# Optimization experiments

Hardware: AMD Instinct MI355X
Metric: run time of the kernel (lower is better)

Reference implementation:

```python
import jax, jax.numpy as jnp
import numpy as np

TEMPERATURE = 0.5
EPS = 1e-8  # matches F.cosine_similarity eps clamp


def setup_inputs() -> dict:
    key = jax.random.key(0)
    k1, k2 = jax.random.split(key)
    logits = jax.random.normal(k1, (8192, 256), dtype=jnp.float32)
    label = jax.random.randint(k2, (8192,), 0, 10, dtype=jnp.int64)
    return {"logits": logits, "label": label}


def reference(logits, label):
    n = label.shape[0]
    # pairwise cosine similarity via normalize + GEMM (same math as the
    # broadcasted F.cosine_similarity, without the O(n^2 d) intermediate)
    norms = jnp.maximum(jnp.linalg.norm(logits, axis=1, keepdims=True), EPS)
    xn = logits / norms                       # [n, d]
    sim_matrix = xn @ xn.T                    # [n, n]

    eye = jnp.eye(n, dtype=sim_matrix.dtype)
    mask = (label[:, None] == label[None, :]).astype(sim_matrix.dtype)  # same-label (incl. diag)

    e = jnp.exp(sim_matrix / TEMPERATURE) * (1.0 - eye)  # zero diagonal
    sim = mask * e                            # same-label positives
    no_sim_sum = jnp.sum(e - sim, axis=1)     # [n] row sums of different-label terms
    sim_sum = sim + no_sim_sum[:, None]       # denominator per entry
    ratio = sim / sim_sum

    # zeros (different-label entries) get +1 via (1 - mask), diagonal gets +1 via eye -> -log(1) = 0
    loss_mat = -jnp.log((1.0 - mask) + ratio + eye)
    return jnp.sum(loss_mat) / (2 * n)
```

## Files before the change

kernel.cpp:

```cpp
#include <hip/hip_runtime.h>
#include <cstdint>
#include <cstddef>

typedef float  f32x4  __attribute__((ext_vector_type(4)));
typedef long long i64;
typedef unsigned char uchar;

#define N_ROWS 8192
#define KDIM   256
#define TEMP_INV 2.0f
#define LOG2E  1.4426950408889634f
#define EXPC   (TEMP_INV * LOG2E)

#define AS1 __attribute__((address_space(1)))
#define AS3 __attribute__((address_space(3)))

__global__ __launch_bounds__(256) void prep(const float* __restrict__ logits,
        const int* __restrict__ label, uchar* __restrict__ xn8,
        int* __restrict__ perm, int* __restrict__ labelPerm,
        int* __restrict__ classStart, int* __restrict__ cumTiles)
{
    __shared__ int lcnt[256][10];
    __shared__ int cstart[11];
    __shared__ int ccount[10];
    const int tid = threadIdx.x;
    const int bid = blockIdx.x;

    if (bid < 2048) {
        const int p = bid * 4 + (tid >> 6);
        const int lane = tid & 63;
        float4 v = reinterpret_cast<const float4*>(logits + (size_t)p * KDIM)[lane];
        float ss = v.x*v.x + v.y*v.y + v.z*v.z + v.w*v.w;
        #pragma unroll
        for (int off = 32; off >= 1; off >>= 1) ss += __shfl_xor(ss, off, 64);
        float inv = 1.0f / fmaxf(sqrtf(ss), 1e-8f);
        int pk = __builtin_amdgcn_cvt_pk_fp8_f32(v.x * inv, v.y * inv, 0, false);
        pk     = __builtin_amdgcn_cvt_pk_fp8_f32(v.z * inv, v.w * inv, pk, true);
        reinterpret_cast<unsigned int*>(xn8 + (size_t)p * KDIM)[lane] = (unsigned int)pk;
        return;
    }

    const int wave = tid >> 6, lane = tid & 63;
    const int beg = tid * 32, end = beg + 32;
    int loc[10] = {0,0,0,0,0,0,0,0,0,0};
    for (int i = beg; i < end; ++i) {
        int c = label[i]; c = (c < 0) ? 0 : (c > 9 ? 9 : c);
        loc[c]++;
    }
    #pragma unroll
    for (int c = 0; c < 10; ++c) lcnt[tid][c] = loc[c];
    __syncthreads();

    for (int c = wave; c < 10; c += 4) {
        int s0 = lcnt[lane*4+0][c], s1 = lcnt[lane*4+1][c];
        int s2 = lcnt[lane*4+2][c], s3 = lcnt[lane*4+3][c];
        int tot = s0 + s1 + s2 + s3;
        int incl = tot;
        #pragma unroll
        for (int d = 1; d < 64; d <<= 1) {
            int up = __shfl_up(incl, d, 64);
            if (lane >= d) incl += up;
        }
        int excl = incl - tot;
        lcnt[lane*4+0][c] = excl;
        lcnt[lane*4+1][c] = excl + s0;
        lcnt[lane*4+2][c] = excl + s0 + s1;
        lcnt[lane*4+3][c] = excl + s0 + s1 + s2;
        if (lane == 63) ccount[c] = incl;
    }
    __syncthreads();

    if (tid == 0) {
        int run = 0, runT = 0;
        for (int c = 0; c < 10; ++c) {
            cstart[c] = run; classStart[c] = run;
            int tpc = (ccount[c] + 127) >> 7;
            cumTiles[c] = runT;
            run  += ccount[c];
            runT += tpc * (tpc + 1) / 2;
        }
        cstart[10] = run; classStart[10] = run; cumTiles[10] = runT;
    }
    __syncthreads();

    int ofs[10];
    #pragma unroll
    for (int c = 0; c < 10; ++c) ofs[c] = lcnt[tid][c];
    for (int i = beg; i < end; ++i) {
        int c = label[i]; c = (c < 0) ? 0 : (c > 9 ? 9 : c);
        int pos = cstart[c] + ofs[c]++;
        perm[pos] = i;
        labelPerm[pos] = c;
    }
}

__device__ __forceinline__ void stage_oneshot(const uchar* __restrict__ xn8,
        const int* __restrict__ perm, int rowBase, int colBase,
        uchar* As, uchar* Bs, int tid)
{
    const int t4 = tid >> 4;
    const int ch = (tid & 15) ^ t4;
    #pragma unroll
    for (int i = 0; i < 8; ++i) {
        const int row = i * 16 + t4;
        int rA = rowBase + row; if (rA > N_ROWS - 1) rA = N_ROWS - 1;
        int rB = colBase + row; if (rB > N_ROWS - 1) rB = N_ROWS - 1;
        const int lds_off = (i * 256 + tid) * 16;
        const uchar* gA = xn8 + (size_t)perm[rA] * KDIM + ch * 16;
        const uchar* gB = xn8 + (size_t)perm[rB] * KDIM + ch * 16;
        __builtin_amdgcn_global_load_lds((const AS1 void*)gA, (AS3 void*)(As + lds_off), 16, 0, 0);
        __builtin_amdgcn_global_load_lds((const AS1 void*)gB, (AS3 void*)(Bs + lds_off), 16, 0, 0);
    }
}

__device__ __forceinline__ void mfma_oneshot(const uchar* As, const uchar* Bs,
        f32x4 (&acc)[4][4], int wave, int lane)
{
    const int wr = wave >> 1, wc = wave & 1;
    const int lrow = lane & 15, kgrp = lane >> 4;
    const int ch2 = kgrp >> 1, half8 = (kgrp & 1) * 8;
    #pragma unroll
    for (int s = 0; s < 8; ++s) {
        const int c16 = s * 2 + ch2;
        i64 a[4], b[4];
        #pragma unroll
        for (int mi = 0; mi < 4; ++mi) {
            const int row = wr*64 + mi*16 + lrow;
            a[mi] = *reinterpret_cast<const i64*>(As + (size_t)row * 256 + ((c16 ^ lrow) * 16) + half8);
        }
        #pragma unroll
        for (int ni = 0; ni < 4; ++ni) {
            const int row = wc*64 + ni*16 + lrow;
            b[ni] = *reinterpret_cast<const i64*>(Bs + (size_t)row * 256 + ((c16 ^ lrow) * 16) + half8);
        }
        #pragma unroll
        for (int mi = 0; mi < 4; ++mi)
            #pragma unroll
            for (int ni = 0; ni < 4; ++ni)
                acc[mi][ni] = __builtin_amdgcn_mfma_f32_16x16x32_fp8_fp8(a[mi], b[ni], acc[mi][ni], 0, 0, 0);
    }
}

__global__ __launch_bounds__(256, 2) void phase1_gemm(const uchar* __restrict__ xn8,
        const int* __restrict__ perm, const int* __restrict__ labelPerm,
        float* __restrict__ pD)
{
    __shared__ __align__(16) char pool[65536];
    uchar* As = (uchar*)(pool);
    uchar* Bs = (uchar*)(pool + 32768);
    float* rowD = (float*)pool;
    float* colD = (float*)(pool + 16384);
    __shared__ int labLDS[256];

    const int tid = threadIdx.x;
    const int wave = tid >> 6, lane = tid & 63;

    int t = blockIdx.x, bi = 0;
    while (t >= 64 - bi) { t -= 64 - bi; ++bi; }
    const int bj = bi + t;
    const bool isDiag = (bi == bj);
    const int rowBase = bi * 128, colBase = bj * 128;

    if (labelPerm[rowBase] == labelPerm[colBase + 127]) {
        if (tid < 128)       pD[(size_t)bj * N_ROWS + rowBase + tid] = 0.f;
        else if (!isDiag)    pD[(size_t)bi * N_ROWS + colBase + tid - 128] = 0.f;
        return;
    }

    stage_oneshot(xn8, perm, rowBase, colBase, As, Bs, tid);
    labLDS[tid] = labelPerm[(tid < 128) ? (rowBase + tid) : (colBase + tid - 128)];
    __syncthreads();

    f32x4 acc[4][4] = {};
    mfma_oneshot(As, Bs, acc, wave, lane);
    __syncthreads();

    const int wr = wave >> 1, wc = wave & 1;
    const int lrow = lane & 15, lgrp = lane >> 4;
    float colAcc[4] = {0.f, 0.f, 0.f, 0.f};
    #pragma unroll
    for (int mi = 0; mi < 4; ++mi) {
        #pragma unroll
        for (int reg = 0; reg < 4; ++reg) {
            const int tr = wr * 64 + mi * 16 + lgrp * 4 + reg;
            const int rl = labLDS[tr];
            float rowAcc = 0.f;
            #pragma unroll
            for (int ni = 0; ni < 4; ++ni) {
                const int tc = wc * 64 + ni * 16 + lrow;
                float e = __builtin_amdgcn_exp2f(acc[mi][ni][reg] * EXPC);
                float ed = (rl != labLDS[128 + tc]) ? e : 0.f;
                rowAcc += ed;
                colAcc[ni] += ed;
            }
            rowD[tr * 32 + wc * 16 + lrow] = rowAcc;
        }
    }
    if (!isDiag) {
        #pragma unroll
        for (int ni = 0; ni < 4; ++ni) {
            const int tc = wc * 64 + ni * 16 + lrow;
            colD[tc * 8 + wr * 4 + lgrp] = colAcc[ni];
        }
    }
    __syncthreads();

    if (tid < 128) {
        const float* p = rowD + tid * 32;
        float s = 0.f;
        #pragma unroll
        for (int k = 0; k < 8; ++k) {
            f32x4 v = *reinterpret_cast<const f32x4*>(p + k * 4);
            s += v[0] + v[1] + v[2] + v[3];
        }
        pD[(size_t)bj * N_ROWS + rowBase + tid] = s;
    } else if (!isDiag) {
        const int c2 = tid - 128;
        const float* p = colD + c2 * 8;
        f32x4 v0 = *reinterpret_cast<const f32x4*>(p);
        f32x4 v1 = *reinterpret_cast<const f32x4*>(p + 4);
        pD[(size_t)bi * N_ROWS + colBase + c2] =
            v0[0] + v0[1] + v0[2] + v0[3] + v1[0] + v1[1] + v1[2] + v1[3];
    }
}

__global__ __launch_bounds__(256, 2) void phase3_loss(const uchar* __restrict__ xn8,
        const int* __restrict__ perm, const float* __restrict__ pD,
        const int* __restrict__ classStart, const int* __restrict__ cumTiles,
        float* __restrict__ partial)
{
    __shared__ __align__(16) char pool[65536];
    uchar* As = (uchar*)(pool);
    uchar* Bs = (uchar*)(pool + 32768);
    __shared__ float redF[256];
    __shared__ float DarrH[256];
    __shared__ float DarrR[128];
    __shared__ float DarrC[128];
    __shared__ int   meta[22];

    const int tid = threadIdx.x;
    const int wave = tid >> 6, lane = tid & 63;

    if (tid < 11) { meta[tid] = classStart[tid]; meta[11 + tid] = cumTiles[tid]; }
    __syncthreads();
    const int nTiles = meta[11 + 10];

    float tileSum = 0.f;
    for (int b = blockIdx.x; b < nTiles; b += 512) {
        __syncthreads();

        int c = 0;
        while (c < 9 && b >= meta[11 + c + 1]) ++c;
        const int s = meta[c], e = meta[c + 1];
        const int nc = e - s;
        const int tps = (nc + 127) >> 7;
        int lt = b - meta[11 + c];
        int ti = 0;
        while (lt >= tps - ti) { lt -= tps - ti; ++ti; }
        const int tj = ti + lt;
        const bool isDiagT = (ti == tj);
        const int rowBase = s + ti * 128, colBase = s + tj * 128;

        stage_oneshot(xn8, perm, rowBase, colBase, As, Bs, tid);

        {
            int r = rowBase + (tid & 127); if (r > N_ROWS - 1) r = N_ROWS - 1;
            const int half = tid >> 7;
            float d = 0.f;
            #pragma unroll 4
            for (int sl = half * 32; sl < half * 32 + 32; ++sl)
                d += pD[(size_t)sl * N_ROWS + r];
            DarrH[(tid & 127) * 2 + half] = d;
        }
        __syncthreads();
        if (tid < 128) DarrR[tid] = DarrH[tid * 2] + DarrH[tid * 2 + 1];
        __syncthreads();
        if (!isDiagT) {
            int r = colBase + (tid & 127); if (r > N_ROWS - 1) r = N_ROWS - 1;
            const int half = tid >> 7;
            float d = 0.f;
            #pragma unroll 4
            for (int sl = half * 32; sl < half * 32 + 32; ++sl)
                d += pD[(size_t)sl * N_ROWS + r];
            DarrH[(tid & 127) * 2 + half] = d;
            __syncthreads();
            if (tid < 128) DarrC[tid] = DarrH[tid * 2] + DarrH[tid * 2 + 1];
        }
        __syncthreads();

        f32x4 acc[4][4] = {};
        mfma_oneshot(As, Bs, acc, wave, lane);

        const int wr = wave >> 1, wc = wave & 1;
        const int lrow = lane & 15, lgrp = lane >> 4;
        #pragma unroll
        for (int mi = 0; mi < 4; ++mi) {
            #pragma unroll
            for (int reg = 0; reg < 4; ++reg) {
                const int tr = wr * 64 + mi * 16 + lgrp * 4 + reg;
                const int r = rowBase + tr;
                if (r < e) {
                    const float Dr = DarrR[tr];
                    #pragma unroll
                    for (int ni = 0; ni < 4; ++ni) {
                        const int tc = wc * 64 + ni * 16 + lrow;
                        const int cg = colBase + tc;
                        if (cg < e) {
                            float sim = acc[mi][ni][reg];
                            float ev = __builtin_amdgcn_exp2f(sim * EXPC);
                            if (isDiagT) {
                                if (cg != r)
                                    tileSum += __logf(ev + Dr) - TEMP_INV * sim;
                            } else {
                                tileSum += __logf(ev + Dr) + __logf(ev + DarrC[tc])
                                         - 2.0f * TEMP_INV * sim;
                            }
                        }
                    }
                }
            }
        }
    }

    __syncthreads();
    redF[tid] = tileSum;
    __syncthreads();
    for (int st = 128; st > 0; st >>= 1) {
        if (tid < st) redF[tid] += redF[tid + st];
        __syncthreads();
    }
    if (tid == 0) partial[blockIdx.x] = redF[0];
}

__global__ void phase4_final(const float* __restrict__ partial, float* __restrict__ out)
{
    __shared__ float red[256];
    const int tid = threadIdx.x;
    float s = partial[tid] + partial[tid + 256];
    red[tid] = s;
    __syncthreads();
    for (int st = 128; st > 0; st >>= 1) {
        if (tid < st) red[tid] += red[tid + st];
        __syncthreads();
    }
    if (tid == 0) out[0] = red[0] * (1.0f / 16384.0f);
}

extern "C" void kernel_launch(void* const* d_in, const int* in_sizes, int n_in,
                              void* d_out, int out_size, void* d_ws, size_t ws_size,
                              hipStream_t stream)
{
    const float* logits = (const float*)d_in[0];
    const int*   label  = (const int*)d_in[1];
    float* out = (float*)d_out;

    char* ws = (char*)d_ws;
    uchar*  xn8       = (uchar*)(ws);
    float*  pD        = (float*)(ws + (2u << 20));
    int*    perm      = (int*)(ws + (4u << 20));
    int*    labelPerm = (int*)(ws + (4u << 20) + (32u << 10));
    int*    classStart= (int*)(ws + (4u << 20) + (64u << 10));
    int*    cumTiles  = (int*)(ws + (4u << 20) + (64u << 10) + 256);
    float*  partial   = (float*)(ws + (4u << 20) + (128u << 10));

    hipLaunchKernelGGL(prep, dim3(2049), dim3(256), 0, stream,
                       logits, label, xn8, perm, labelPerm, classStart, cumTiles);
    hipLaunchKernelGGL(phase1_gemm, dim3(2080), dim3(256), 0, stream,
                       xn8, perm, labelPerm, pD);
    hipLaunchKernelGGL(phase3_loss, dim3(512), dim3(256), 0, stream,
                       xn8, perm, pD, classStart, cumTiles, partial);
    hipLaunchKernelGGL(phase4_final, dim3(1), dim3(256), 0, stream,
                       partial, out);
}
```

Measured before the change: 67.97 us.

## Enlarge phase1 GEMM tiles to 256x256 with 512-thread blocks

The phase1 symmetric GEMM moves from 128x128 tiles with 256 threads to 256x256 tiles with 512 threads (8 waves, each computing a 128x64 block), using 128KB of LDS per block. The grid drops from 2080 to 528 upper-triangle tiles, so pD holds 32 column slices instead of 64, and phase3 now sums 32 slices. The aim is to halve the global loads per FLOP and cut per-block overhead. In exchange, occupancy falls to one block per CU, there are fewer blocks to spread across the CUs, and the same-label skip check is coarser, so fewer tiles can be skipped.

```diff
diff --git a/kernel.cpp b/kernel.cpp
--- a/kernel.cpp
+++ b/kernel.cpp
@@ -91,6 +91,127 @@
         int pos = cstart[c] + ofs[c]++;
         perm[pos] = i;
         labelPerm[pos] = c;
+    }
+}
+
+__device__ __forceinline__ void stage_quad(const uchar* __restrict__ xn8,
+        const int* __restrict__ perm, int rowBase, int colBase,
+        uchar* As, uchar* Bs, int tid)
+{
+    const int t5 = tid >> 4;
+    const int ch = (tid & 15) ^ (t5 & 15);
+    #pragma unroll
+    for (int i = 0; i < 8; ++i) {
+        const int row = i * 32 + t5;
+        const int lds_off = (i * 512 + tid) * 16;
+        const uchar* gA = xn8 + (size_t)perm[rowBase + row] * KDIM + ch * 16;
+        const uchar* gB = xn8 + (size_t)perm[colBase + row] * KDIM + ch * 16;
+        __builtin_amdgcn_global_load_lds((const AS1 void*)gA, (AS3 void*)(As + lds_off), 16, 0, 0);
+        __builtin_amdgcn_global_load_lds((const AS1 void*)gB, (AS3 void*)(Bs + lds_off), 16, 0, 0);
+    }
+}
+
+__global__ __launch_bounds__(512, 1) void phase1_gemm(const uchar* __restrict__ xn8,
+        const int* __restrict__ perm, const int* __restrict__ labelPerm,
+        float* __restrict__ pD)
+{
+    __shared__ __align__(16) char pool[131072];
+    uchar* As = (uchar*)(pool);
+    uchar* Bs = (uchar*)(pool + 65536);
+    float* rowD = (float*)pool;
+    float* colD = (float*)(pool + 65536);
+    __shared__ int labq[512];
+
+    const int tid = threadIdx.x;
+    const int wave = tid >> 6, lane = tid & 63;
+
+    int t = blockIdx.x, Bi = 0;
+    while (t >= 32 - Bi) { t -= 32 - Bi; ++Bi; }
+    const int Bj = Bi + t;
+    const bool isDiag = (Bi == Bj);
+    const int rowBase = Bi * 256, colBase = Bj * 256;
+
+    if (labelPerm[rowBase] == labelPerm[colBase + 255]) {
+        if (tid < 256)       pD[(size_t)Bj * N_ROWS + rowBase + tid] = 0.f;
+        else if (!isDiag)    pD[(size_t)Bi * N_ROWS + colBase + tid - 256] = 0.f;
+        return;
+    }
+
+    stage_quad(xn8, perm, rowBase, colBase, As, Bs, tid);
+    labq[tid] = labelPerm[(tid < 256) ? (rowBase + tid) : (colBase + tid - 256)];
+    __syncthreads();
+
+    const int wr = wave >> 2, wc = wave & 3;
+    const int lrow = lane & 15, kgrp = lane >> 4;
+    const int ch2 = kgrp >> 1, half8 = (kgrp & 1) * 8;
+    f32x4 acc[8][4] = {};
+    #pragma unroll
+    for (int s = 0; s < 8; ++s) {
+        const int c16 = s * 2 + ch2;
+        i64 a[8], b[4];
+        #pragma unroll
+        for (int mi = 0; mi < 8; ++mi) {
+            const int row = wr*128 + mi*16 + lrow;
+            a[mi] = *reinterpret_cast<const i64*>(As + (size_t)row * 256 + ((c16 ^ lrow) * 16) + half8);
+        }
+        #pragma unroll
+        for (int ni = 0; ni < 4; ++ni) {
+            const int row = wc*64 + ni*16 + lrow;
+            b[ni] = *reinterpret_cast<const i64*>(Bs + (size_t)row * 256 + ((c16 ^ lrow) * 16) + half8);
+        }
+        #pragma unroll
+        for (int mi = 0; mi < 8; ++mi)
+            #pragma unroll
+            for (int ni = 0; ni < 4; ++ni)
+                acc[mi][ni] = __builtin_amdgcn_mfma_f32_16x16x32_fp8_fp8(a[mi], b[ni], acc[mi][ni], 0, 0, 0);
+    }
+    __syncthreads();
+
+    const int lgrp = lane >> 4;
+    float colAcc[4] = {0.f, 0.f, 0.f, 0.f};
+    #pragma unroll
+    for (int mi = 0; mi < 8; ++mi) {
+        #pragma unroll
+        for (int reg = 0; reg < 4; ++reg) {
+            const int tr = wr * 128 + mi * 16 + lgrp * 4 + reg;
+            const int rl = labq[tr];
+            float rowAcc = 0.f;
+            #pragma unroll
+            for (int ni = 0; ni < 4; ++ni) {
+                const int tc = wc * 64 + ni * 16 + lrow;
+                float e = __builtin_amdgcn_exp2f(acc[mi][ni][reg] * EXPC);
+                float ed = (rl != labq[256 + tc]) ? e : 0.f;
+                rowAcc += ed;
+                colAcc[ni] += ed;
+            }
+            rowD[tr * 64 + wc * 16 + lrow] = rowAcc;
+        }
+    }
+    if (!isDiag) {
+        #pragma unroll
+        for (int ni = 0; ni < 4; ++ni) {
+            const int tc = wc * 64 + ni * 16 + lrow;
+            colD[tc * 8 + wr * 4 + lgrp] = colAcc[ni];
+        }
+    }
+    __syncthreads();
+
+    if (tid < 256) {
+        const float* p = rowD + tid * 64;
+        float s = 0.f;
+        #pragma unroll
+        for (int k = 0; k < 16; ++k) {
+            f32x4 v = *reinterpret_cast<const f32x4*>(p + k * 4);
+            s += v[0] + v[1] + v[2] + v[3];
+        }
+        pD[(size_t)Bj * N_ROWS + rowBase + tid] = s;
+    } else if (!isDiag) {
+        const int c2 = tid - 256;
+        const float* p = colD + c2 * 8;
+        f32x4 v0 = *reinterpret_cast<const f32x4*>(p);
+        f32x4 v1 = *reinterpret_cast<const f32x4*>(p + 4);
+        pD[(size_t)Bi * N_ROWS + colBase + c2] =
+            v0[0] + v0[1] + v0[2] + v0[3] + v1[0] + v1[1] + v1[2] + v1[3];
     }
 }
 
@@ -138,89 +259,6 @@
             #pragma unroll
             for (int ni = 0; ni < 4; ++ni)
                 acc[mi][ni] = __builtin_amdgcn_mfma_f32_16x16x32_fp8_fp8(a[mi], b[ni], acc[mi][ni], 0, 0, 0);
-    }
-}
-
-__global__ __launch_bounds__(256, 2) void phase1_gemm(const uchar* __restrict__ xn8,
-        const int* __restrict__ perm, const int* __restrict__ labelPerm,
-        float* __restrict__ pD)
-{
-    __shared__ __align__(16) char pool[65536];
-    uchar* As = (uchar*)(pool);
-    uchar* Bs = (uchar*)(pool + 32768);
-    float* rowD = (float*)pool;
-    float* colD = (float*)(pool + 16384);
-    __shared__ int labLDS[256];
-
-    const int tid = threadIdx.x;
-    const int wave = tid >> 6, lane = tid & 63;
-
-    int t = blockIdx.x, bi = 0;
-    while (t >= 64 - bi) { t -= 64 - bi; ++bi; }
-    const int bj = bi + t;
-    const bool isDiag = (bi == bj);
-    const int rowBase = bi * 128, colBase = bj * 128;
-
-    if (labelPerm[rowBase] == labelPerm[colBase + 127]) {
-        if (tid < 128)       pD[(size_t)bj * N_ROWS + rowBase + tid] = 0.f;
-        else if (!isDiag)    pD[(size_t)bi * N_ROWS + colBase + tid - 128] = 0.f;
-        return;
-    }
-
-    stage_oneshot(xn8, perm, rowBase, colBase, As, Bs, tid);
-    labLDS[tid] = labelPerm[(tid < 128) ? (rowBase + tid) : (colBase + tid - 128)];
-    __syncthreads();
-
-    f32x4 acc[4][4] = {};
-    mfma_oneshot(As, Bs, acc, wave, lane);
-    __syncthreads();
-
-    const int wr = wave >> 1, wc = wave & 1;
-    const int lrow = lane & 15, lgrp = lane >> 4;
-    float colAcc[4] = {0.f, 0.f, 0.f, 0.f};
-    #pragma unroll
-    for (int mi = 0; mi < 4; ++mi) {
-        #pragma unroll
-        for (int reg = 0; reg < 4; ++reg) {
-            const int tr = wr * 64 + mi * 16 + lgrp * 4 + reg;
-            const int rl = labLDS[tr];
-            float rowAcc = 0.f;
-            #pragma unroll
-            for (int ni = 0; ni < 4; ++ni) {
-                const int tc = wc * 64 + ni * 16 + lrow;
-                float e = __builtin_amdgcn_exp2f(acc[mi][ni][reg] * EXPC);
-                float ed = (rl != labLDS[128 + tc]) ? e : 0.f;
-                rowAcc += ed;
-                colAcc[ni] += ed;
-            }
-            rowD[tr * 32 + wc * 16 + lrow] = rowAcc;
-        }
-    }
-    if (!isDiag) {
-        #pragma unroll
-        for (int ni = 0; ni < 4; ++ni) {
-            const int tc = wc * 64 + ni * 16 + lrow;
-            colD[tc * 8 + wr * 4 + lgrp] = colAcc[ni];
-        }
-    }
-    __syncthreads();
-
-    if (tid < 128) {
-        const float* p = rowD + tid * 32;
-        float s = 0.f;
-        #pragma unroll
-        for (int k = 0; k < 8; ++k) {
-            f32x4 v = *reinterpret_cast<const f32x4*>(p + k * 4);
-            s += v[0] + v[1] + v[2] + v[3];
-        }
-        pD[(size_t)bj * N_ROWS + rowBase + tid] = s;
-    } else if (!isDiag) {
-        const int c2 = tid - 128;
-        const float* p = colD + c2 * 8;
-        f32x4 v0 = *reinterpret_cast<const f32x4*>(p);
-        f32x4 v1 = *reinterpret_cast<const f32x4*>(p + 4);
-        pD[(size_t)bi * N_ROWS + colBase + c2] =
-            v0[0] + v0[1] + v0[2] + v0[3] + v1[0] + v1[1] + v1[2] + v1[3];
     }
 }
 
@@ -268,7 +306,7 @@
             const int half = tid >> 7;
             float d = 0.f;
             #pragma unroll 4
-            for (int sl = half * 32; sl < half * 32 + 32; ++sl)
+            for (int sl = half * 16; sl < half * 16 + 16; ++sl)
                 d += pD[(size_t)sl * N_ROWS + r];
             DarrH[(tid & 127) * 2 + half] = d;
         }
@@ -280,7 +318,7 @@
             const int half = tid >> 7;
             float d = 0.f;
             #pragma unroll 4
-            for (int sl = half * 32; sl < half * 32 + 32; ++sl)
+            for (int sl = half * 16; sl < half * 16 + 16; ++sl)
                 d += pD[(size_t)sl * N_ROWS + r];
             DarrH[(tid & 127) * 2 + half] = d;
             __syncthreads();
@@ -365,7 +403,7 @@
 
     hipLaunchKernelGGL(prep, dim3(2049), dim3(256), 0, stream,
                        logits, label, xn8, perm, labelPerm, classStart, cumTiles);
-    hipLaunchKernelGGL(phase1_gemm, dim3(2080), dim3(256), 0, stream,
+    hipLaunchKernelGGL(phase1_gemm, dim3(528), dim3(512), 0, stream,
                        xn8, perm, labelPerm, pD);
     hipLaunchKernelGGL(phase3_loss, dim3(512), dim3(256), 0, stream,
                        xn8, perm, pD, classStart, cumTiles, partial);
```

Result: slower. 74.07 us (+9.0%).

## Split K staging into two halves to halve LDS and raise occupancy

Applied to the files above, without the earlier changes.

The GEMM tiles in both the phase1 and phase3 kernels now stage A and B in two K-halves of 128 bytes instead of one 256-byte shot. This halves the LDS pool to 32KB and raises launch bounds from 2 to 4 blocks per CU. The swizzle changes to an 8-chunk XOR pattern to match the new row pitch. In exchange, each tile adds two extra barriers and a load phase with no overlap between them, and any latency hiding must now come from the extra resident blocks.

```diff
diff --git a/kernel.cpp b/kernel.cpp
--- a/kernel.cpp
+++ b/kernel.cpp
@@ -94,44 +94,44 @@
     }
 }
 
-__device__ __forceinline__ void stage_oneshot(const uchar* __restrict__ xn8,
-        const int* __restrict__ perm, int rowBase, int colBase,
+__device__ __forceinline__ void stage_half(const uchar* __restrict__ xn8,
+        const int* __restrict__ perm, int rowBase, int colBase, int kb,
         uchar* As, uchar* Bs, int tid)
 {
-    const int t4 = tid >> 4;
-    const int ch = (tid & 15) ^ t4;
-    #pragma unroll
-    for (int i = 0; i < 8; ++i) {
-        const int row = i * 16 + t4;
+    #pragma unroll
+    for (int i = 0; i < 4; ++i) {
+        const int ci = i * 256 + tid;
+        const int row = ci >> 3;
+        const int c = (ci & 7) ^ (row & 7);
         int rA = rowBase + row; if (rA > N_ROWS - 1) rA = N_ROWS - 1;
         int rB = colBase + row; if (rB > N_ROWS - 1) rB = N_ROWS - 1;
-        const int lds_off = (i * 256 + tid) * 16;
-        const uchar* gA = xn8 + (size_t)perm[rA] * KDIM + ch * 16;
-        const uchar* gB = xn8 + (size_t)perm[rB] * KDIM + ch * 16;
+        const int lds_off = ci * 16;
+        const uchar* gA = xn8 + (size_t)perm[rA] * KDIM + kb + c * 16;
+        const uchar* gB = xn8 + (size_t)perm[rB] * KDIM + kb + c * 16;
         __builtin_amdgcn_global_load_lds((const AS1 void*)gA, (AS3 void*)(As + lds_off), 16, 0, 0);
         __builtin_amdgcn_global_load_lds((const AS1 void*)gB, (AS3 void*)(Bs + lds_off), 16, 0, 0);
     }
 }
 
-__device__ __forceinline__ void mfma_oneshot(const uchar* As, const uchar* Bs,
+__device__ __forceinline__ void mfma_half(const uchar* As, const uchar* Bs,
         f32x4 (&acc)[4][4], int wave, int lane)
 {
     const int wr = wave >> 1, wc = wave & 1;
     const int lrow = lane & 15, kgrp = lane >> 4;
     const int ch2 = kgrp >> 1, half8 = (kgrp & 1) * 8;
     #pragma unroll
-    for (int s = 0; s < 8; ++s) {
+    for (int s = 0; s < 4; ++s) {
         const int c16 = s * 2 + ch2;
         i64 a[4], b[4];
         #pragma unroll
         for (int mi = 0; mi < 4; ++mi) {
             const int row = wr*64 + mi*16 + lrow;
-            a[mi] = *reinterpret_cast<const i64*>(As + (size_t)row * 256 + ((c16 ^ lrow) * 16) + half8);
+            a[mi] = *reinterpret_cast<const i64*>(As + (size_t)row * 128 + ((c16 ^ (row & 7)) * 16) + half8);
         }
         #pragma unroll
         for (int ni = 0; ni < 4; ++ni) {
             const int row = wc*64 + ni*16 + lrow;
-            b[ni] = *reinterpret_cast<const i64*>(Bs + (size_t)row * 256 + ((c16 ^ lrow) * 16) + half8);
+            b[ni] = *reinterpret_cast<const i64*>(Bs + (size_t)row * 128 + ((c16 ^ (row & 7)) * 16) + half8);
         }
         #pragma unroll
         for (int mi = 0; mi < 4; ++mi)
@@ -141,13 +141,13 @@
     }
 }
 
-__global__ __launch_bounds__(256, 2) void phase1_gemm(const uchar* __restrict__ xn8,
+__global__ __launch_bounds__(256, 4) void phase1_gemm(const uchar* __restrict__ xn8,
         const int* __restrict__ perm, const int* __restrict__ labelPerm,
         float* __restrict__ pD)
 {
-    __shared__ __align__(16) char pool[65536];
+    __shared__ __align__(16) char pool[32768];
     uchar* As = (uchar*)(pool);
-    uchar* Bs = (uchar*)(pool + 32768);
+    uchar* Bs = (uchar*)(pool + 16384);
     float* rowD = (float*)pool;
     float* colD = (float*)(pool + 16384);
     __shared__ int labLDS[256];
@@ -167,12 +167,16 @@
         return;
     }
 
-    stage_oneshot(xn8, perm, rowBase, colBase, As, Bs, tid);
+    stage_half(xn8, perm, rowBase, colBase, 0, As, Bs, tid);
     labLDS[tid] = labelPerm[(tid < 128) ? (rowBase + tid) : (colBase + tid - 128)];
     __syncthreads();
 
     f32x4 acc[4][4] = {};
-    mfma_oneshot(As, Bs, acc, wave, lane);
+    mfma_half(As, Bs, acc, wave, lane);
+    __syncthreads();
+    stage_half(xn8, perm, rowBase, colBase, 128, As, Bs, tid);
+    __syncthreads();
+    mfma_half(As, Bs, acc, wave, lane);
     __syncthreads();
 
     const int wr = wave >> 1, wc = wave & 1;
@@ -224,14 +228,14 @@
     }
 }
 
-__global__ __launch_bounds__(256, 2) void phase3_loss(const uchar* __restrict__ xn8,
+__global__ __launch_bounds__(256, 4) void phase3_loss(const uchar* __restrict__ xn8,
         const int* __restrict__ perm, const float* __restrict__ pD,
         const int* __restrict__ classStart, const int* __restrict__ cumTiles,
         float* __restrict__ partial)
 {
-    __shared__ __align__(16) char pool[65536];
+    __shared__ __align__(16) char pool[32768];
     uchar* As = (uchar*)(pool);
-    uchar* Bs = (uchar*)(pool + 32768);
+    uchar* Bs = (uchar*)(pool + 16384);
     __shared__ float redF[256];
     __shared__ float DarrH[256];
     __shared__ float DarrR[128];
@@ -261,7 +265,7 @@
         const bool isDiagT = (ti == tj);
         const int rowBase = s + ti * 128, colBase = s + tj * 128;
 
-        stage_oneshot(xn8, perm, rowBase, colBase, As, Bs, tid);
+        stage_half(xn8, perm, rowBase, colBase, 0, As, Bs, tid);
 
         {
             int r = rowBase + (tid & 127); if (r > N_ROWS - 1) r = N_ROWS - 1;
@@ -289,7 +293,11 @@
         __syncthreads();
 
         f32x4 acc[4][4] = {};
-        mfma_oneshot(As, Bs, acc, wave, lane);
+        mfma_half(As, Bs, acc, wave, lane);
+        __syncthreads();
+        stage_half(xn8, perm, rowBase, colBase, 128, As, Bs, tid);
+        __syncthreads();
+        mfma_half(As, Bs, acc, wave, lane);
 
         const int wr = wave >> 1, wc = wave & 1;
         const int lrow = lane & 15, lgrp = lane >> 4;
```

Result: slower. 71.56 us (+5.3%).

## Pair column tiles per block to reuse row tile and overlap staging

Applied to the files above, without the earlier changes.

Each phase1 block now handles two adjacent column tiles that share one staged row tile, halving the grid. The second B tile is loaded while the first tile's epilogue runs, and row and column partial sums are reduced with wave shuffles instead of large LDS scratch arrays. The prep label pass now uses a strided, register-cached layout, which changes the stable order within each class. The risk is fewer blocks to fill the GPU and longer serial work per block.

```diff
diff --git a/kernel.cpp b/kernel.cpp
--- a/kernel.cpp
+++ b/kernel.cpp
@@ -41,12 +41,15 @@
     }
 
     const int wave = tid >> 6, lane = tid & 63;
-    const int beg = tid * 32, end = beg + 32;
+    int lab[32];
+    #pragma unroll
+    for (int j = 0; j < 32; ++j) {
+        int c = label[tid + j * 256];
+        lab[j] = (c < 0) ? 0 : (c > 9 ? 9 : c);
+    }
     int loc[10] = {0,0,0,0,0,0,0,0,0,0};
-    for (int i = beg; i < end; ++i) {
-        int c = label[i]; c = (c < 0) ? 0 : (c > 9 ? 9 : c);
-        loc[c]++;
-    }
+    #pragma unroll
+    for (int j = 0; j < 32; ++j) loc[lab[j]]++;
     #pragma unroll
     for (int c = 0; c < 10; ++c) lcnt[tid][c] = loc[c];
     __syncthreads();
@@ -86,12 +89,166 @@
     int ofs[10];
     #pragma unroll
     for (int c = 0; c < 10; ++c) ofs[c] = lcnt[tid][c];
-    for (int i = beg; i < end; ++i) {
-        int c = label[i]; c = (c < 0) ? 0 : (c > 9 ? 9 : c);
+    #pragma unroll
+    for (int j = 0; j < 32; ++j) {
+        int c = lab[j];
         int pos = cstart[c] + ofs[c]++;
-        perm[pos] = i;
+        perm[pos] = tid + j * 256;
         labelPerm[pos] = c;
     }
+}
+
+__device__ __forceinline__ void stage_mat(const uchar* __restrict__ xn8,
+        const int* __restrict__ perm, int base, uchar* dst, int tid)
+{
+    const int t4 = tid >> 4;
+    const int ch = (tid & 15) ^ t4;
+    #pragma unroll
+    for (int i = 0; i < 8; ++i) {
+        const int row = i * 16 + t4;
+        const int lds_off = (i * 256 + tid) * 16;
+        const uchar* g = xn8 + (size_t)perm[base + row] * KDIM + ch * 16;
+        __builtin_amdgcn_global_load_lds((const AS1 void*)g, (AS3 void*)(dst + lds_off), 16, 0, 0);
+    }
+}
+
+__device__ __forceinline__ void mfma_oneshot(const uchar* As, const uchar* Bs,
+        f32x4 (&acc)[4][4], int wave, int lane)
+{
+    const int wr = wave >> 1, wc = wave & 1;
+    const int lrow = lane & 15, kgrp = lane >> 4;
+    const int ch2 = kgrp >> 1, half8 = (kgrp & 1) * 8;
+    #pragma unroll
+    for (int s = 0; s < 8; ++s) {
+        const int c16 = s * 2 + ch2;
+        i64 a[4], b[4];
+        #pragma unroll
+        for (int mi = 0; mi < 4; ++mi) {
+            const int row = wr*64 + mi*16 + lrow;
+            a[mi] = *reinterpret_cast<const i64*>(As + (size_t)row * 256 + ((c16 ^ lrow) * 16) + half8);
+        }
+        #pragma unroll
+        for (int ni = 0; ni < 4; ++ni) {
+            const int row = wc*64 + ni*16 + lrow;
+            b[ni] = *reinterpret_cast<const i64*>(Bs + (size_t)row * 256 + ((c16 ^ lrow) * 16) + half8);
+        }
+        #pragma unroll
+        for (int mi = 0; mi < 4; ++mi)
+            #pragma unroll
+            for (int ni = 0; ni < 4; ++ni)
+                acc[mi][ni] = __builtin_amdgcn_mfma_f32_16x16x32_fp8_fp8(a[mi], b[ni], acc[mi][ni], 0, 0, 0);
+    }
+}
+
+__device__ __forceinline__ void epilogue_reg(f32x4 (&acc)[4][4],
+        const int* labR, const int* labC, float (*rowHalf)[2], float (*colHalf)[2],
+        int wave, int lane)
+{
+    const int wr = wave >> 1, wc = wave & 1;
+    const int lrow = lane & 15, lgrp = lane >> 4;
+    float colAcc[4] = {0.f, 0.f, 0.f, 0.f};
+    #pragma unroll
+    for (int mi = 0; mi < 4; ++mi) {
+        #pragma unroll
+        for (int reg = 0; reg < 4; ++reg) {
+            const int tr = wr * 64 + mi * 16 + lgrp * 4 + reg;
+            const int rl = labR[tr];
+            float rowAcc = 0.f;
+            #pragma unroll
+            for (int ni = 0; ni < 4; ++ni) {
+                const int tc = wc * 64 + ni * 16 + lrow;
+                float e = __builtin_amdgcn_exp2f(acc[mi][ni][reg] * EXPC);
+                float ed = (rl != labC[tc]) ? e : 0.f;
+                rowAcc += ed;
+                colAcc[ni] += ed;
+            }
+            #pragma unroll
+            for (int off = 1; off < 16; off <<= 1)
+                rowAcc += __shfl_xor(rowAcc, off, 64);
+            if (lrow == 0) rowHalf[tr][wc] = rowAcc;
+        }
+    }
+    #pragma unroll
+    for (int ni = 0; ni < 4; ++ni) {
+        colAcc[ni] += __shfl_xor(colAcc[ni], 16, 64);
+        colAcc[ni] += __shfl_xor(colAcc[ni], 32, 64);
+        if (lgrp == 0) colHalf[wc * 64 + ni * 16 + lrow][wr] = colAcc[ni];
+    }
+}
+
+__global__ __launch_bounds__(256, 2) void phase1_gemm(const uchar* __restrict__ xn8,
+        const int* __restrict__ perm, const int* __restrict__ labelPerm,
+        float* __restrict__ pD)
+{
+    __shared__ __align__(16) uchar As[32768];
+    __shared__ __align__(16) uchar Bs[32768];
+    __shared__ float rowHalf[128][2];
+    __shared__ float colHalf[128][2];
+    __shared__ int labAll[384];
+
+    const int tid = threadIdx.x;
+    const int wave = tid >> 6, lane = tid & 63;
+
+    int t = blockIdx.x, bi = 0;
+    while (t >= ((65 - bi) >> 1)) { t -= (65 - bi) >> 1; ++bi; }
+    const int bj0 = bi + 2 * t;
+    const bool hasT1 = (bj0 + 1) < 64;
+    const int bj1 = hasT1 ? (bj0 + 1) : bj0;
+    const int rowBase = bi * 128, colBase0 = bj0 * 128, colBase1 = bj1 * 128;
+    const bool isDiag0 = (bi == bj0);
+
+    const int rl0 = labelPerm[rowBase];
+    const bool same0 = (rl0 == labelPerm[colBase0 + 127]);
+    const bool same1 = !hasT1 || (rl0 == labelPerm[colBase1 + 127]);
+
+    if (same0 && same1) {
+        if (tid < 128) {
+            pD[(size_t)bj0 * N_ROWS + rowBase + tid] = 0.f;
+            if (hasT1) pD[(size_t)bj1 * N_ROWS + rowBase + tid] = 0.f;
+        } else {
+            if (!isDiag0) pD[(size_t)bi * N_ROWS + colBase0 + tid - 128] = 0.f;
+            if (hasT1)    pD[(size_t)bi * N_ROWS + colBase1 + tid - 128] = 0.f;
+        }
+        return;
+    }
+
+    stage_mat(xn8, perm, rowBase, As, tid);
+    if (!same0) stage_mat(xn8, perm, colBase0, Bs, tid);
+    labAll[tid] = labelPerm[(tid < 128) ? (rowBase + tid) : (colBase0 + tid - 128)];
+    if (tid < 128) labAll[256 + tid] = labelPerm[colBase1 + tid];
+    __syncthreads();
+
+    f32x4 acc[4][4] = {};
+    if (!same0) mfma_oneshot(As, Bs, acc, wave, lane);
+    __syncthreads();
+
+    if (hasT1 && !same1) stage_mat(xn8, perm, colBase1, Bs, tid);
+    if (!same0)
+        epilogue_reg(acc, labAll, labAll + 128, rowHalf, colHalf, wave, lane);
+    __syncthreads();
+
+    if (tid < 128)
+        pD[(size_t)bj0 * N_ROWS + rowBase + tid] =
+            same0 ? 0.f : (rowHalf[tid][0] + rowHalf[tid][1]);
+    else if (!isDiag0)
+        pD[(size_t)bi * N_ROWS + colBase0 + tid - 128] =
+            same0 ? 0.f : (colHalf[tid - 128][0] + colHalf[tid - 128][1]);
+
+    if (!hasT1) return;
+
+    f32x4 acc1[4][4] = {};
+    if (!same1) mfma_oneshot(As, Bs, acc1, wave, lane);
+    __syncthreads();
+    if (!same1)
+        epilogue_reg(acc1, labAll, labAll + 256, rowHalf, colHalf, wave, lane);
+    __syncthreads();
+
+    if (tid < 128)
+        pD[(size_t)bj1 * N_ROWS + rowBase + tid] =
+            same1 ? 0.f : (rowHalf[tid][0] + rowHalf[tid][1]);
+    else
+        pD[(size_t)bi * N_ROWS + colBase1 + tid - 128] =
+            same1 ? 0.f : (colHalf[tid - 128][0] + colHalf[tid - 128][1]);
 }
 
 __device__ __forceinline__ void stage_oneshot(const uchar* __restrict__ xn8,
@@ -110,117 +267,6 @@
         const uchar* gB = xn8 + (size_t)perm[rB] * KDIM + ch * 16;
         __builtin_amdgcn_global_load_lds((const AS1 void*)gA, (AS3 void*)(As + lds_off), 16, 0, 0);
         __builtin_amdgcn_global_load_lds((const AS1 void*)gB, (AS3 void*)(Bs + lds_off), 16, 0, 0);
-    }
-}
-
-__device__ __forceinline__ void mfma_oneshot(const uchar* As, const uchar* Bs,
-        f32x4 (&acc)[4][4], int wave, int lane)
-{
-    const int wr = wave >> 1, wc = wave & 1;
-    const int lrow = lane & 15, kgrp = lane >> 4;
-    const int ch2 = kgrp >> 1, half8 = (kgrp & 1) * 8;
-    #pragma unroll
-    for (int s = 0; s < 8; ++s) {
-        const int c16 = s * 2 + ch2;
-        i64 a[4], b[4];
-        #pragma unroll
-        for (int mi = 0; mi < 4; ++mi) {
-            const int row = wr*64 + mi*16 + lrow;
-            a[mi] = *reinterpret_cast<const i64*>(As + (size_t)row * 256 + ((c16 ^ lrow) * 16) + half8);
-        }
-        #pragma unroll
-        for (int ni = 0; ni < 4; ++ni) {
-            const int row = wc*64 + ni*16 + lrow;
-            b[ni] = *reinterpret_cast<const i64*>(Bs + (size_t)row * 256 + ((c16 ^ lrow) * 16) + half8);
-        }
-        #pragma unroll
-        for (int mi = 0; mi < 4; ++mi)
-            #pragma unroll
-            for (int ni = 0; ni < 4; ++ni)
-                acc[mi][ni] = __builtin_amdgcn_mfma_f32_16x16x32_fp8_fp8(a[mi], b[ni], acc[mi][ni], 0, 0, 0);
-    }
-}
-
-__global__ __launch_bounds__(256, 2) void phase1_gemm(const uchar* __restrict__ xn8,
-        const int* __restrict__ perm, const int* __restrict__ labelPerm,
-        float* __restrict__ pD)
-{
-    __shared__ __align__(16) char pool[65536];
-    uchar* As = (uchar*)(pool);
-    uchar* Bs = (uchar*)(pool + 32768);
-    float* rowD = (float*)pool;
-    float* colD = (float*)(pool + 16384);
-    __shared__ int labLDS[256];
-
-    const int tid = threadIdx.x;
-    const int wave = tid >> 6, lane = tid & 63;
-
-    int t = blockIdx.x, bi = 0;
-    while (t >= 64 - bi) { t -= 64 - bi; ++bi; }
-    const int bj = bi + t;
-    const bool isDiag = (bi == bj);
-    const int rowBase = bi * 128, colBase = bj * 128;
-
-    if (labelPerm[rowBase] == labelPerm[colBase + 127]) {
-        if (tid < 128)       pD[(size_t)bj * N_ROWS + rowBase + tid] = 0.f;
-        else if (!isDiag)    pD[(size_t)bi * N_ROWS + colBase + tid - 128] = 0.f;
-        return;
-    }
-
-    stage_oneshot(xn8, perm, rowBase, colBase, As, Bs, tid);
-    labLDS[tid] = labelPerm[(tid < 128) ? (rowBase + tid) : (colBase + tid - 128)];
-    __syncthreads();
-
-    f32x4 acc[4][4] = {};
-    mfma_oneshot(As, Bs, acc, wave, lane);
-    __syncthreads();
-
-    const int wr = wave >> 1, wc = wave & 1;
-    const int lrow = lane & 15, lgrp = lane >> 4;
-    float colAcc[4] = {0.f, 0.f, 0.f, 0.f};
-    #pragma unroll
-    for (int mi = 0; mi < 4; ++mi) {
-        #pragma unroll
-        for (int reg = 0; reg < 4; ++reg) {
-            const int tr = wr * 64 + mi * 16 + lgrp * 4 + reg;
-            const int rl = labLDS[tr];
-            float rowAcc = 0.f;
-            #pragma unroll
-            for (int ni = 0; ni < 4; ++ni) {
-                const int tc = wc * 64 + ni * 16 + lrow;
-                float e = __builtin_amdgcn_exp2f(acc[mi][ni][reg] * EXPC);
-                float ed = (rl != labLDS[128 + tc]) ? e : 0.f;
-                rowAcc += ed;
-                colAcc[ni] += ed;
-            }
-            rowD[tr * 32 + wc * 16 + lrow] = rowAcc;
-        }
-    }
-    if (!isDiag) {
-        #pragma unroll
-        for (int ni = 0; ni < 4; ++ni) {
-            const int tc = wc * 64 + ni * 16 + lrow;
-            colD[tc * 8 + wr * 4 + lgrp] = colAcc[ni];
-        }
-    }
-    __syncthreads();
-
-    if (tid < 128) {
-        const float* p = rowD + tid * 32;
-        float s = 0.f;
-        #pragma unroll
-        for (int k = 0; k < 8; ++k) {
-            f32x4 v = *reinterpret_cast<const f32x4*>(p + k * 4);
-            s += v[0] + v[1] + v[2] + v[3];
-        }
-        pD[(size_t)bj * N_ROWS + rowBase + tid] = s;
-    } else if (!isDiag) {
-        const int c2 = tid - 128;
-        const float* p = colD + c2 * 8;
-        f32x4 v0 = *reinterpret_cast<const f32x4*>(p);
-        f32x4 v1 = *reinterpret_cast<const f32x4*>(p + 4);
-        pD[(size_t)bi * N_ROWS + colBase + c2] =
-            v0[0] + v0[1] + v0[2] + v0[3] + v1[0] + v1[1] + v1[2] + v1[3];
     }
 }
 
@@ -365,7 +411,7 @@
 
     hipLaunchKernelGGL(prep, dim3(2049), dim3(256), 0, stream,
                        logits, label, xn8, perm, labelPerm, classStart, cumTiles);
-    hipLaunchKernelGGL(phase1_gemm, dim3(2080), dim3(256), 0, stream,
+    hipLaunchKernelGGL(phase1_gemm, dim3(1056), dim3(256), 0, stream,
                        xn8, perm, labelPerm, pD);
     hipLaunchKernelGGL(phase3_loss, dim3(512), dim3(256), 0, stream,
                        xn8, perm, pD, classStart, cumTiles, partial);
```

Result: slower. 79.36 us (+16.7%).
